# Kernel optimization log

Hardware: AMD Instinct MI355X
Metric: run time of the kernel (lower is better)

Reference implementation:

```python
import jax, jax.numpy as jnp
import numpy as np

N = 500000      # active voxels
C_IN = 16       # input voxel feature dim
# encoder channels per stage: 32, 64, 128


def setup_inputs() -> dict:
    key = jax.random.key(0)
    ks = jax.random.split(key, 16)

    def w(k, i, o):
        return jax.random.normal(k, (i, o), dtype=jnp.float32) * (1.0 / np.sqrt(i))

    d = {}
    d['feat'] = jax.random.normal(ks[0], (N, C_IN), dtype=jnp.float32)
    d['coords'] = jax.random.randint(ks[1], (N, 4), 0, 1024, dtype=jnp.int32)
    d['W_in'] = w(ks[2], C_IN, 32)
    d['W_enc1'] = w(ks[3], 32, 32)
    d['W_enc2'] = w(ks[4], 32, 64)
    d['W_enc3'] = w(ks[5], 64, 128)
    d['W_lat1'] = w(ks[6], 32, 32)
    d['W_lat2'] = w(ks[7], 64, 64)
    d['W_lat3'] = w(ks[8], 128, 128)
    d['W_merge1'] = w(ks[9], 64, 32)    # merge: 2*C_i -> C_i
    d['W_merge2'] = w(ks[10], 128, 64)
    d['W_merge3'] = w(ks[11], 256, 128)
    d['W_up1'] = w(ks[12], 32, 32)      # upsample: C_i -> C_{i-1}
    d['W_up2'] = w(ks[13], 64, 32)
    d['W_up3'] = w(ks[14], 128, 64)
    return d


def _forward(feat, W_in, W_enc1, W_enc2, W_enc3, W_lat1, W_lat2, W_lat3,
             W_merge1, W_merge2, W_merge3, W_up1, W_up2, W_up3):
    relu = jax.nn.relu
    # conv_input + encoder (1x1 submanifold sparse convs == per-voxel matmul)
    x = relu(feat @ W_in)
    e1 = relu(x @ W_enc1)
    e2 = relu(e1 @ W_enc2)
    e3 = relu(e2 @ W_enc3)
    enc = [e1, e2, e3]
    lats = [W_lat1, W_lat2, W_lat3]
    mrgs = [W_merge1, W_merge2, W_merge3]
    ups = [W_up1, W_up2, W_up3]
    x = e3
    for i in (2, 1, 0):  # decoder stages stage_num..1
        lat = relu(enc[i] @ lats[i])                    # lateral_layer
        # cat0(x_bottom) + cat1(lat): identity-placement 1x1 convs == concat
        cat = jnp.concatenate([x, lat], axis=-1)        # [N, 2*C_i]
        merge = relu(cat @ mrgs[i])                     # merge_layer 2C->C
        red = cat.reshape(cat.shape[0], -1, 2).sum(-1)  # reduce_channel: fixed pairwise-sum conv
        x = relu((merge + red) @ ups[i])                # residual add + upsample_layer
    return x  # ret['voxel_feats']


def reference(feat, coords, W_in, W_enc1, W_enc2, W_enc3, W_lat1, W_lat2, W_lat3,
              W_merge1, W_merge2, W_merge3, W_up1, W_up2, W_up3):
    # coords define sparse structure; for 1x1 subm convs the math only touches features
    return _forward(feat, W_in, W_enc1, W_enc2, W_enc3, W_lat1, W_lat2, W_lat3,
                    W_merge1, W_merge2, W_merge3, W_up1, W_up2, W_up3)
```

## Files before the change

### kernel.cpp

```cpp
#include <hip/hip_runtime.h>

typedef unsigned short u16;
typedef unsigned int u32;
typedef _Float16 h16;
typedef __attribute__((ext_vector_type(4))) _Float16 half4;
typedef __attribute__((ext_vector_type(8))) _Float16 half8;
typedef __attribute__((ext_vector_type(8))) unsigned short ushort8;
typedef __attribute__((ext_vector_type(4))) float f32x4;

#define NPAIRS 15625
#define STRIPO 11648

#define AE1 0
#define SE1 72
#define AE2 1152
#define SE2 136
#define ACT 3328
#define SCT 520
#define AMR 3584
#define SMR 520

#define MFMA16(A,B,C) __builtin_amdgcn_mfma_f32_16x16x32_f16(A,B,C,0,0,0)

#define LBAR() asm volatile("s_waitcnt lgkmcnt(0)\n\ts_barrier" ::: "memory")

#define F_L0   0
#define F_L1   2
#define F_L2   4
#define F_L3   8
#define F_L4   24
#define F_L5   56
#define F_L6   120
#define F_L7   136
#define F_L8   144
#define F_L9   160
#define F_L10  164
#define F_L11  166
#define F_L12  170
#define NFRAG  172

__device__ __forceinline__ u16 hb(h16 h) { union { h16 h; u16 u; } v; v.h = h; return v.u; }

__global__ __launch_bounds__(256) void pack_w(
    const float* w0, const float* w1, const float* w2, const float* w3, const float* w4,
    const float* w5, const float* w6, const float* w7, const float* w8, const float* w9,
    const float* w10, const float* w11, const float* w12, u16* __restrict__ packed)
{
  const float* ws[13] = {w0,w1,w2,w3,w4,w5,w6,w7,w8,w9,w10,w11,w12};
  const int Ka[13]  = {16,32,32,64,128,256,128,64,128,64,32,64,32};
  const int KT[13]  = {1,1,1,2,4,8,4,2,4,2,1,2,1};
  const int CO[13]  = {32,32,64,128,128,128,64,64,64,32,32,32,32};
  const int FO[13]  = {F_L0,F_L1,F_L2,F_L3,F_L4,F_L5,F_L6,F_L7,F_L8,F_L9,F_L10,F_L11,F_L12};
  int g = blockIdx.x * 256 + threadIdx.x;
  int f = g >> 6, lane = g & 63;
  if (f >= NFRAG) return;
  int layer = 0;
#pragma unroll
  for (int i = 1; i < 13; ++i) if (f >= FO[i]) layer = i;
  int fl = f - FO[layer];
  int kt = fl % KT[layer];
  int ct = fl / KT[layer];
  int cout = CO[layer];
  int quad = lane >> 4;
  int col  = ct * 16 + (lane & 15);
  u16 thi[8], tlo[8];
#pragma unroll
  for (int j = 0; j < 8; ++j) {
    int k = kt * 32 + quad * 8 + j;
    float w = (k < Ka[layer]) ? ws[layer][k * cout + col] : 0.f;
    h16 h = (h16)w;
    h16 l = (h16)(w - (float)h);
    thi[j] = hb(h); tlo[j] = hb(l);
  }
  u16* dst = packed + ((size_t)f * 64 + lane) * 16;
  *(ushort8*)dst       = *(const ushort8*)thi;
  *(ushort8*)(dst + 8) = *(const ushort8*)tlo;
}


__device__ __forceinline__ void packw(h16* dst, int idx2, float v) {
  h16 h = (h16)v;
  h16 l = (h16)(v - (float)h);
  union { u16 s[2]; u32 u; } z;
  z.s[0] = hb(h); z.s[1] = hb(l);
  *reinterpret_cast<u32*>(dst + idx2) = z.u;
}

__device__ __forceinline__ float red2i(const h16* cat, int cs, int rr, int cc) {
  half4 v = *reinterpret_cast<const half4*>(cat + rr * cs + 4 * cc);
  return (float)v.x + (float)v.y + (float)v.z + (float)v.w;
}

template<int KT, int EPI, int BAR>
__device__ __forceinline__ void layerW(
    const h16* __restrict__ asrc, int as,
    const h16* __restrict__ wp, int foff, int ct, int lane,
    half8 pbh, half8 pbl,
    h16* dst, int ds, int colb, const h16* cat, int cs,
    float* __restrict__ gout, int row0)
{
  const int l15 = lane & 15, quad = lane >> 4;
  const int abase = l15 * as + quad * 16;
  f32x4 a0 = {0.f,0.f,0.f,0.f}, a1 = {0.f,0.f,0.f,0.f};
#pragma unroll
  for (int kt = 0; kt < KT; ++kt) {
    half8 bhv, blv;
    if (kt == 0) { bhv = pbh; blv = pbl; }
    else {
      const h16* fp = wp + (((size_t)(foff + ct * KT + kt)) * 64 + lane) * 16;
      bhv = *(const half8*)fp;
      blv = *(const half8*)(fp + 8);
    }
    const h16* p0 = asrc + abase + kt * 64;
    const h16* p1 = p0 + STRIPO;
    half8 q0a = *(const half8*)p0, q0b = *(const half8*)(p0 + 8);
    half8 q1a = *(const half8*)p1, q1b = *(const half8*)(p1 + 8);
    half8 ah0 = __builtin_shufflevector(q0a, q0b, 0,2,4,6,8,10,12,14);
    half8 al0 = __builtin_shufflevector(q0a, q0b, 1,3,5,7,9,11,13,15);
    half8 ah1 = __builtin_shufflevector(q1a, q1b, 0,2,4,6,8,10,12,14);
    half8 al1 = __builtin_shufflevector(q1a, q1b, 1,3,5,7,9,11,13,15);
    a0 = MFMA16(al0, bhv, a0); a0 = MFMA16(ah0, blv, a0); a0 = MFMA16(ah0, bhv, a0);
    a1 = MFMA16(al1, bhv, a1); a1 = MFMA16(ah1, blv, a1); a1 = MFMA16(ah1, bhv, a1);
  }
  const int cc = ct * 16 + l15;
  float v0r[4], v1r[4];
#pragma unroll
  for (int r = 0; r < 4; ++r) {
    const int rr = quad * 4 + r;
    float v0 = a0[r] > 0.f ? a0[r] : 0.f;
    float v1 = a1[r] > 0.f ? a1[r] : 0.f;
    if (EPI == 1) {
      v0 += red2i(cat, cs, rr, cc);
      v1 += red2i(cat + STRIPO, cs, rr, cc);
    }
    v0r[r] = v0; v1r[r] = v1;
  }
  if (BAR) LBAR();
  if (EPI <= 1) {
#pragma unroll
    for (int r = 0; r < 4; ++r) {
      const int rr = quad * 4 + r;
      const int idx2 = rr * ds + 2 * (colb + cc);
      packw(dst, idx2, v0r[r]);
      packw(dst + STRIPO, idx2, v1r[r]);
    }
  } else {
#pragma unroll
    for (int r = 0; r < 4; ++r) {
      const int rr = quad * 4 + r;
      gout[(size_t)(row0 + rr) * 32 + cc]      = v0r[r];
      gout[(size_t)(row0 + 16 + rr) * 32 + cc] = v1r[r];
    }
  }
}

#define PFB(FOFF, CIDX, KT_)                                                        \
  do { const h16* _fp = wp + (((size_t)((FOFF) + (CIDX) * (KT_))) * 64 + lane) * 16; \
       pbh = *(const half8*)_fp; pbl = *(const half8*)(_fp + 8); } while (0)

__global__ __launch_bounds__(512, 6) void backbone(
    const float* __restrict__ feat, const h16* __restrict__ wp, float* __restrict__ out)
{
  __shared__ h16 lds[2 * STRIPO];
  const int lane = threadIdx.x & 63;
  const int wv   = threadIdx.x >> 6;
  const int l15 = lane & 15, quad = lane >> 4;
  const int row0 = blockIdx.x * 32;

  h16* E1 = lds + AE1;
  h16* E2 = lds + AE2;
  h16* CT = lds + ACT;
  h16* MR = lds + AMR;

  half8 pbh, pbl;

  if (wv < 2) {
    PFB(F_L0, wv, 1);
    h16 th0[8] = {0,0,0,0,0,0,0,0}, tl0[8] = {0,0,0,0,0,0,0,0};
    h16 th1[8] = {0,0,0,0,0,0,0,0}, tl1[8] = {0,0,0,0,0,0,0,0};
    if (quad < 2) {
      const float* s0 = feat + (size_t)(row0 + l15) * 16 + quad * 8;
      const float* s1 = feat + (size_t)(row0 + 16 + l15) * 16 + quad * 8;
      f32x4 u0a = *(const f32x4*)s0, u0b = *(const f32x4*)(s0 + 4);
      f32x4 u1a = *(const f32x4*)s1, u1b = *(const f32x4*)(s1 + 4);
#pragma unroll
      for (int j = 0; j < 4; ++j) {
        h16 h;
        h = (h16)u0a[j]; th0[j]   = h; tl0[j]   = (h16)(u0a[j] - (float)h);
        h = (h16)u0b[j]; th0[4+j] = h; tl0[4+j] = (h16)(u0b[j] - (float)h);
        h = (h16)u1a[j]; th1[j]   = h; tl1[j]   = (h16)(u1a[j] - (float)h);
        h = (h16)u1b[j]; th1[4+j] = h; tl1[4+j] = (h16)(u1b[j] - (float)h);
      }
    }
    half8 ah0 = *(const half8*)th0, al0 = *(const half8*)tl0;
    half8 ah1 = *(const half8*)th1, al1 = *(const half8*)tl1;
    f32x4 a0 = {0.f,0.f,0.f,0.f}, a1 = {0.f,0.f,0.f,0.f};
    a0 = MFMA16(al0, pbh, a0); a0 = MFMA16(ah0, pbl, a0); a0 = MFMA16(ah0, pbh, a0);
    a1 = MFMA16(al1, pbh, a1); a1 = MFMA16(ah1, pbl, a1); a1 = MFMA16(ah1, pbh, a1);
#pragma unroll
    for (int r = 0; r < 4; ++r) {
      const int rr = quad * 4 + r;
      const int idx2 = rr * SCT + 2 * (wv * 16 + l15);
      packw(CT,          idx2, a0[r] > 0.f ? a0[r] : 0.f);
      packw(CT + STRIPO, idx2, a1[r] > 0.f ? a1[r] : 0.f);
    }
    PFB(F_L1, wv, 1);
  }
  LBAR();

  if (wv < 2) {
    layerW<1,0,0>(CT,SCT, wp, F_L1, wv, lane, pbh,pbl, E1,SE1,0, nullptr,0, nullptr,0);
  }
  if (wv < 4) PFB(F_L2, wv, 1);
  LBAR();

  if (wv < 4) {
    layerW<1,0,0>(E1,SE1, wp, F_L2, wv, lane, pbh,pbl, E2,SE2,0, nullptr,0, nullptr,0);
  }
  PFB(F_L3, wv, 2);
  LBAR();

  layerW<2,0,0>(E2,SE2, wp, F_L3, wv, lane, pbh,pbl, CT,SCT,0, nullptr,0, nullptr,0);
  PFB(F_L4, wv, 4);
  LBAR();

  layerW<4,0,0>(CT,SCT, wp, F_L4, wv, lane, pbh,pbl, CT,SCT,128, nullptr,0, nullptr,0);
  PFB(F_L5, wv, 8);
  LBAR();

  layerW<8,1,1>(CT,SCT, wp, F_L5, wv, lane, pbh,pbl, MR,SMR,0, CT,SCT, nullptr,0);
  if (wv < 4) PFB(F_L6, wv, 4); else PFB(F_L7, wv - 4, 2);
  LBAR();

  if (wv < 4) {
    layerW<4,0,0>(MR,SMR, wp, F_L6, wv, lane, pbh,pbl, CT,SCT,0,  nullptr,0, nullptr,0);
  } else {
    layerW<2,0,0>(E2,SE2, wp, F_L7, wv - 4, lane, pbh,pbl, CT,SCT,64, nullptr,0, nullptr,0);
  }
  if (wv < 4) PFB(F_L8, wv, 4);
  LBAR();

  if (wv < 4) {
    layerW<4,1,0>(CT,SCT, wp, F_L8, wv, lane, pbh,pbl, MR,SMR,0, CT,SCT, nullptr,0);
  }
  if (wv < 2) PFB(F_L9, wv, 2);
  else if (wv < 4) PFB(F_L10, wv - 2, 1);
  LBAR();

  if (wv < 2) {
    layerW<2,0,0>(MR,SMR, wp, F_L9, wv, lane, pbh,pbl, CT,SCT,0,  nullptr,0, nullptr,0);
  } else if (wv < 4) {
    layerW<1,0,0>(E1,SE1, wp, F_L10, wv - 2, lane, pbh,pbl, CT,SCT,32, nullptr,0, nullptr,0);
  }
  if (wv < 2) PFB(F_L11, wv, 2);
  LBAR();

  if (wv < 2) {
    layerW<2,1,0>(CT,SCT, wp, F_L11, wv, lane, pbh,pbl, MR,SMR,0, CT,SCT, nullptr,0);
    PFB(F_L12, wv, 1);
  }
  LBAR();

  if (wv < 2) {
    layerW<1,2,0>(MR,SMR, wp, F_L12, wv, lane, pbh,pbl, nullptr,0,0, nullptr,0, out, row0);
  }
}

extern "C" void kernel_launch(void* const* d_in, const int* in_sizes, int n_in,
                              void* d_out, int out_size, void* d_ws, size_t ws_size,
                              hipStream_t stream) {
  (void)in_sizes; (void)n_in; (void)out_size; (void)ws_size;
  u16* packed = (u16*)d_ws;

  hipLaunchKernelGGL(pack_w, dim3(43), dim3(256), 0, stream,
      (const float*)d_in[2],  (const float*)d_in[3],  (const float*)d_in[4],
      (const float*)d_in[5],  (const float*)d_in[8],  (const float*)d_in[11],
      (const float*)d_in[14], (const float*)d_in[7],  (const float*)d_in[10],
      (const float*)d_in[13], (const float*)d_in[6],  (const float*)d_in[9],
      (const float*)d_in[12], packed);

  hipLaunchKernelGGL(backbone, dim3(NPAIRS), dim3(512), 0, stream,
                     (const float*)d_in[0], (const h16*)packed, (float*)d_out);
}
```

Baseline: 449.1 us.

## Store hi/lo fp16 split activations in separate LDS planes instead of interleaved

Changes the LDS activation layout from interleaved hi/lo fp16 pairs to separate hi and lo row planes (rows offset by 16*stride), with new strides and offsets. A-operand loads become two direct half8 reads with no shuffle deinterleave, and the pairwise-sum epilogue reads half2 from both planes. Stores become two 16-bit writes instead of one packed 32-bit write, which may raise LDS store count and bank behavior changes.

New measurement: 432.3 us. -3.7%, faster.

```diff
diff --git a/kernel.cpp b/kernel.cpp
--- a/kernel.cpp
+++ b/kernel.cpp
@@ -3,22 +3,22 @@
 typedef unsigned short u16;
 typedef unsigned int u32;
 typedef _Float16 h16;
-typedef __attribute__((ext_vector_type(4))) _Float16 half4;
+typedef __attribute__((ext_vector_type(2))) _Float16 half2v;
 typedef __attribute__((ext_vector_type(8))) _Float16 half8;
 typedef __attribute__((ext_vector_type(8))) unsigned short ushort8;
 typedef __attribute__((ext_vector_type(4))) float f32x4;
 
 #define NPAIRS 15625
-#define STRIPO 11648
+#define STRIPH 12032
 
 #define AE1 0
-#define SE1 72
-#define AE2 1152
-#define SE2 136
-#define ACT 3328
-#define SCT 520
-#define AMR 3584
-#define SMR 520
+#define SE1 40
+#define AE2 1280
+#define SE2 72
+#define ACT 3584
+#define SCT 264
+#define AMR 3712
+#define SMR 264
 
 #define MFMA16(A,B,C) __builtin_amdgcn_mfma_f32_16x16x32_f16(A,B,C,0,0,0)
 
@@ -78,17 +78,16 @@
 }
 
 
-__device__ __forceinline__ void packw(h16* dst, int idx2, float v) {
+__device__ __forceinline__ void splitw(h16* dst, int idx, int dlo, float v) {
   h16 h = (h16)v;
-  h16 l = (h16)(v - (float)h);
-  union { u16 s[2]; u32 u; } z;
-  z.s[0] = hb(h); z.s[1] = hb(l);
-  *reinterpret_cast<u32*>(dst + idx2) = z.u;
-}
-
-__device__ __forceinline__ float red2i(const h16* cat, int cs, int rr, int cc) {
-  half4 v = *reinterpret_cast<const half4*>(cat + rr * cs + 4 * cc);
-  return (float)v.x + (float)v.y + (float)v.z + (float)v.w;
+  dst[idx]       = h;
+  dst[idx + dlo] = (h16)(v - (float)h);
+}
+
+__device__ __forceinline__ float red2p(const h16* cat, int cs, int rr, int cc) {
+  half2v hp = *reinterpret_cast<const half2v*>(cat + rr * cs + 2 * cc);
+  half2v lp = *reinterpret_cast<const half2v*>(cat + (rr + 16) * cs + 2 * cc);
+  return (float)hp.x + (float)hp.y + (float)lp.x + (float)lp.y;
 }
 
 template<int KT, int EPI, int BAR>
@@ -100,7 +99,8 @@
     float* __restrict__ gout, int row0)
 {
   const int l15 = lane & 15, quad = lane >> 4;
-  const int abase = l15 * as + quad * 16;
+  const int abase = l15 * as + quad * 8;
+  const int alo = 16 * as;
   f32x4 a0 = {0.f,0.f,0.f,0.f}, a1 = {0.f,0.f,0.f,0.f};
 #pragma unroll
   for (int kt = 0; kt < KT; ++kt) {
@@ -111,14 +111,12 @@
       bhv = *(const half8*)fp;
       blv = *(const half8*)(fp + 8);
     }
-    const h16* p0 = asrc + abase + kt * 64;
-    const h16* p1 = p0 + STRIPO;
-    half8 q0a = *(const half8*)p0, q0b = *(const half8*)(p0 + 8);
-    half8 q1a = *(const half8*)p1, q1b = *(const half8*)(p1 + 8);
-    half8 ah0 = __builtin_shufflevector(q0a, q0b, 0,2,4,6,8,10,12,14);
-    half8 al0 = __builtin_shufflevector(q0a, q0b, 1,3,5,7,9,11,13,15);
-    half8 ah1 = __builtin_shufflevector(q1a, q1b, 0,2,4,6,8,10,12,14);
-    half8 al1 = __builtin_shufflevector(q1a, q1b, 1,3,5,7,9,11,13,15);
+    const h16* p0 = asrc + abase + kt * 32;
+    const h16* p1 = p0 + STRIPH;
+    half8 ah0 = *(const half8*)p0;
+    half8 al0 = *(const half8*)(p0 + alo);
+    half8 ah1 = *(const half8*)p1;
+    half8 al1 = *(const half8*)(p1 + alo);
     a0 = MFMA16(al0, bhv, a0); a0 = MFMA16(ah0, blv, a0); a0 = MFMA16(ah0, bhv, a0);
     a1 = MFMA16(al1, bhv, a1); a1 = MFMA16(ah1, blv, a1); a1 = MFMA16(ah1, bhv, a1);
   }
@@ -130,19 +128,20 @@
     float v0 = a0[r] > 0.f ? a0[r] : 0.f;
     float v1 = a1[r] > 0.f ? a1[r] : 0.f;
     if (EPI == 1) {
-      v0 += red2i(cat, cs, rr, cc);
-      v1 += red2i(cat + STRIPO, cs, rr, cc);
+      v0 += red2p(cat, cs, rr, cc);
+      v1 += red2p(cat + STRIPH, cs, rr, cc);
     }
     v0r[r] = v0; v1r[r] = v1;
   }
   if (BAR) LBAR();
   if (EPI <= 1) {
+    const int dlo = 16 * ds;
 #pragma unroll
     for (int r = 0; r < 4; ++r) {
       const int rr = quad * 4 + r;
-      const int idx2 = rr * ds + 2 * (colb + cc);
-      packw(dst, idx2, v0r[r]);
-      packw(dst + STRIPO, idx2, v1r[r]);
+      const int idx = rr * ds + colb + cc;
+      splitw(dst,          idx, dlo, v0r[r]);
+      splitw(dst + STRIPH, idx, dlo, v1r[r]);
     }
   } else {
 #pragma unroll
@@ -161,7 +160,7 @@
 __global__ __launch_bounds__(512, 6) void backbone(
     const float* __restrict__ feat, const h16* __restrict__ wp, float* __restrict__ out)
 {
-  __shared__ h16 lds[2 * STRIPO];
+  __shared__ h16 lds[2 * STRIPH];
   const int lane = threadIdx.x & 63;
   const int wv   = threadIdx.x >> 6;
   const int l15 = lane & 15, quad = lane >> 4;
@@ -197,12 +196,13 @@
     f32x4 a0 = {0.f,0.f,0.f,0.f}, a1 = {0.f,0.f,0.f,0.f};
     a0 = MFMA16(al0, pbh, a0); a0 = MFMA16(ah0, pbl, a0); a0 = MFMA16(ah0, pbh, a0);
     a1 = MFMA16(al1, pbh, a1); a1 = MFMA16(ah1, pbl, a1); a1 = MFMA16(ah1, pbh, a1);
+    const int dlo = 16 * SCT;
 #pragma unroll
     for (int r = 0; r < 4; ++r) {
       const int rr = quad * 4 + r;
-      const int idx2 = rr * SCT + 2 * (wv * 16 + l15);
-      packw(CT,          idx2, a0[r] > 0.f ? a0[r] : 0.f);
-      packw(CT + STRIPO, idx2, a1[r] > 0.f ? a1[r] : 0.f);
+      const int idx = rr * SCT + wv * 16 + l15;
+      splitw(CT,          idx, dlo, a0[r] > 0.f ? a0[r] : 0.f);
+      splitw(CT + STRIPH, idx, dlo, a1[r] > 0.f ? a1[r] : 0.f);
     }
     PFB(F_L1, wv, 1);
   }
```
